# Kernel tuning notes

Measured on AMD Instinct MI355X. Metric: run time of the kernel, lower is better.

Reference implementation:

```python
import jax, jax.numpy as jnp
import numpy as np


def setup_inputs() -> dict:
    key = jax.random.key(0)
    k1, k2, k3, k4, k5 = jax.random.split(key, 5)
    C, S = 256, 16  # in_channels, se_channels
    x = jax.random.normal(k1, (64, C, 56, 56), dtype=jnp.float32)
    # 1x1 conv weights stored as [out, in] (kernel spatial dims are 1x1)
    w1 = jax.random.normal(k2, (S, C), dtype=jnp.float32) * (1.0 / np.sqrt(C))
    b1 = jax.random.normal(k3, (S,), dtype=jnp.float32) * 0.01
    w2 = jax.random.normal(k4, (C, S), dtype=jnp.float32) * (1.0 / np.sqrt(S))
    b2 = jax.random.normal(k5, (C,), dtype=jnp.float32) * 0.01
    return {"x": x, "w1": w1, "b1": b1, "w2": w2, "b2": b2}


def reference(x, w1, b1, w2, b2):
    # squeeze: global average pool over H, W -> [N, C]
    s = jnp.mean(x, axis=(2, 3))
    # excitation: 1x1 conv MLP with swish then sigmoid gate
    h = jnp.einsum('nc,sc->ns', s, w1) + b1          # [N, S]
    h = h * jax.nn.sigmoid(h)                        # swish
    g = jax.nn.sigmoid(jnp.einsum('ns,cs->nc', h, w2) + b2)  # [N, C]
    # broadcast multiply back over spatial dims
    return x * g[:, :, None, None]
```

## Files before the change

### kernel.cpp

```cpp
#include <hip/hip_runtime.h>
#include <math.h>

#define N_   64
#define C_   256
#define S_   16
#define HW_  3136
#define HW4_ 784
#define ROWS_ (N_ * C_)
#define BLK_  4096

typedef float f32x4 __attribute__((ext_vector_type(4)));

__device__ __forceinline__ float sigmoidf_(float v) {
    return 1.0f / (1.0f + expf(-v));
}

__global__ __launch_bounds__(256) void se_pool(const float* __restrict__ x,
                                               float* __restrict__ s) {
    const int wave = threadIdx.x >> 6;
    const int lane = threadIdx.x & 63;
    const int row  = blockIdx.x * 4 + wave;
    const f32x4* xr = reinterpret_cast<const f32x4*>(x + (size_t)row * HW_);

    f32x4 acc = {0.f, 0.f, 0.f, 0.f};
    #pragma unroll
    for (int u = 0; u < 12; ++u) acc += xr[lane + 64 * u];
    float sum = (acc.x + acc.y) + (acc.z + acc.w);
    if (lane < 16) {
        f32x4 v = xr[768 + lane];
        sum += (v.x + v.y) + (v.z + v.w);
    }
    #pragma unroll
    for (int off = 32; off; off >>= 1) sum += __shfl_down(sum, off, 64);
    if (lane == 0) s[row] = sum * (1.0f / (float)HW_);
}

__global__ __launch_bounds__(256) void se_mlp(const float* __restrict__ s,
                                              const float* __restrict__ w1,
                                              const float* __restrict__ b1,
                                              const float* __restrict__ w2,
                                              const float* __restrict__ b2,
                                              float* __restrict__ g) {
    const int n = blockIdx.x;
    const int t = threadIdx.x;
    __shared__ float s_sh[C_];
    __shared__ float h_sh[S_];
    s_sh[t] = s[n * C_ + t];
    __syncthreads();

    const int j  = t >> 4;
    const int sl = t & 15;
    float p = 0.f;
    #pragma unroll
    for (int k = sl; k < C_; k += 16) p += s_sh[k] * w1[j * C_ + k];
    #pragma unroll
    for (int m = 8; m; m >>= 1) p += __shfl_xor(p, m, 64);
    if (sl == 0) {
        float hv = p + b1[j];
        h_sh[j] = hv * sigmoidf_(hv);
    }
    __syncthreads();

    float acc = b2[t];
    #pragma unroll
    for (int k = 0; k < S_; ++k) acc += h_sh[k] * w2[t * S_ + k];
    g[n * C_ + t] = sigmoidf_(acc);
}

__global__ __launch_bounds__(256) void se_scale(const float* __restrict__ x,
                                                const float* __restrict__ g,
                                                float* __restrict__ out) {
    const int wave = threadIdx.x >> 6;
    const int lane = threadIdx.x & 63;
    const int row  = blockIdx.x * 4 + wave;
    const float gv = g[row];
    const f32x4* xr = reinterpret_cast<const f32x4*>(x + (size_t)row * HW_);
    f32x4* orow = reinterpret_cast<f32x4*>(out + (size_t)row * HW_);

    #pragma unroll
    for (int u = 0; u < 12; ++u) {
        f32x4 v = xr[lane + 64 * u];
        v *= gv;
        __builtin_nontemporal_store(v, &orow[lane + 64 * u]);
    }
    if (lane < 16) {
        f32x4 v = xr[768 + lane];
        v *= gv;
        __builtin_nontemporal_store(v, &orow[768 + lane]);
    }
}

extern "C" void kernel_launch(void* const* d_in, const int* in_sizes, int n_in,
                              void* d_out, int out_size, void* d_ws, size_t ws_size,
                              hipStream_t stream) {
    const float* x  = (const float*)d_in[0];
    const float* w1 = (const float*)d_in[1];
    const float* b1 = (const float*)d_in[2];
    const float* w2 = (const float*)d_in[3];
    const float* b2 = (const float*)d_in[4];
    float* out = (float*)d_out;

    float* s = (float*)d_ws;
    float* g = s + ROWS_;

    se_pool <<<BLK_, 256, 0, stream>>>(x, s);
    se_mlp  <<<N_,   256, 0, stream>>>(s, w1, b1, w2, b2, g);
    se_scale<<<BLK_, 256, 0, stream>>>(x, g, out);
}
```

Baseline: 99.91 us.

## Fuse SE excitation MLP into scale kernel, recomputing gate per wave

Removes the separate small MLP kernel by having each wave in the scale kernel recompute the gate for its (n,c) row from the pooled vector, w1, and w2 with shuffle reductions. The x loads are issued into registers before the MLP math so their latency overlaps the gate computation. This eliminates one kernel launch and the serialization of a low-occupancy 64-block kernel. In exchange, every wave redundantly computes the full 16x256 first layer, which adds ALU work, L2 traffic for s and w1, and register pressure from holding 13 vectors of x.

Result: slower. 112.4 us (+12.5%).

```diff
diff --git a/kernel.cpp b/kernel.cpp
--- a/kernel.cpp
+++ b/kernel.cpp
@@ -35,57 +35,53 @@
     if (lane == 0) s[row] = sum * (1.0f / (float)HW_);
 }
 
-__global__ __launch_bounds__(256) void se_mlp(const float* __restrict__ s,
-                                              const float* __restrict__ w1,
-                                              const float* __restrict__ b1,
-                                              const float* __restrict__ w2,
-                                              const float* __restrict__ b2,
-                                              float* __restrict__ g) {
-    const int n = blockIdx.x;
-    const int t = threadIdx.x;
-    __shared__ float s_sh[C_];
-    __shared__ float h_sh[S_];
-    s_sh[t] = s[n * C_ + t];
-    __syncthreads();
-
-    const int j  = t >> 4;
-    const int sl = t & 15;
-    float p = 0.f;
-    #pragma unroll
-    for (int k = sl; k < C_; k += 16) p += s_sh[k] * w1[j * C_ + k];
-    #pragma unroll
-    for (int m = 8; m; m >>= 1) p += __shfl_xor(p, m, 64);
-    if (sl == 0) {
-        float hv = p + b1[j];
-        h_sh[j] = hv * sigmoidf_(hv);
-    }
-    __syncthreads();
-
-    float acc = b2[t];
-    #pragma unroll
-    for (int k = 0; k < S_; ++k) acc += h_sh[k] * w2[t * S_ + k];
-    g[n * C_ + t] = sigmoidf_(acc);
-}
-
-__global__ __launch_bounds__(256) void se_scale(const float* __restrict__ x,
-                                                const float* __restrict__ g,
-                                                float* __restrict__ out) {
+__global__ __launch_bounds__(256) void se_gate_scale(
+    const float* __restrict__ x, const float* __restrict__ s,
+    const float* __restrict__ w1, const float* __restrict__ b1,
+    const float* __restrict__ w2, const float* __restrict__ b2,
+    float* __restrict__ out)
+{
     const int wave = threadIdx.x >> 6;
     const int lane = threadIdx.x & 63;
     const int row  = blockIdx.x * 4 + wave;
-    const float gv = g[row];
+    const int n    = row >> 8;
+    const int c    = row & (C_ - 1);
     const f32x4* xr = reinterpret_cast<const f32x4*>(x + (size_t)row * HW_);
+
+    f32x4 xv[12];
+    #pragma unroll
+    for (int u = 0; u < 12; ++u) xv[u] = xr[lane + 64 * u];
+    f32x4 xt = {0.f, 0.f, 0.f, 0.f};
+    if (lane < 16) xt = xr[768 + lane];
+
+    const int j   = lane >> 2;
+    const int seg = lane & 3;
+    const f32x4* s4 = reinterpret_cast<const f32x4*>(s  + n * C_ + seg * 64);
+    const f32x4* w4 = reinterpret_cast<const f32x4*>(w1 + j * C_ + seg * 64);
+    f32x4 pa = {0.f, 0.f, 0.f, 0.f};
+    #pragma unroll
+    for (int m = 0; m < 16; ++m) pa += s4[m] * w4[m];
+    float p = (pa.x + pa.y) + (pa.z + pa.w);
+    p += __shfl_xor(p, 1, 64);
+    p += __shfl_xor(p, 2, 64);
+    float hv = p + b1[j];
+    hv = hv * sigmoidf_(hv);
+
+    float term = (seg == 0) ? hv * w2[c * S_ + j] : 0.f;
+    term += __shfl_xor(term, 4,  64);
+    term += __shfl_xor(term, 8,  64);
+    term += __shfl_xor(term, 16, 64);
+    term += __shfl_xor(term, 32, 64);
+    const float gv = sigmoidf_(__shfl(term, 0, 64) + b2[c]);
+
     f32x4* orow = reinterpret_cast<f32x4*>(out + (size_t)row * HW_);
-
     #pragma unroll
     for (int u = 0; u < 12; ++u) {
-        f32x4 v = xr[lane + 64 * u];
-        v *= gv;
+        f32x4 v = xv[u] * gv;
         __builtin_nontemporal_store(v, &orow[lane + 64 * u]);
     }
     if (lane < 16) {
-        f32x4 v = xr[768 + lane];
-        v *= gv;
+        f32x4 v = xt * gv;
         __builtin_nontemporal_store(v, &orow[768 + lane]);
     }
 }
@@ -101,9 +97,7 @@
     float* out = (float*)d_out;
 
     float* s = (float*)d_ws;
-    float* g = s + ROWS_;
 
-    se_pool <<<BLK_, 256, 0, stream>>>(x, s);
-    se_mlp  <<<N_,   256, 0, stream>>>(s, w1, b1, w2, b2, g);
-    se_scale<<<BLK_, 256, 0, stream>>>(x, g, out);
+    se_pool      <<<BLK_, 256, 0, stream>>>(x, s);
+    se_gate_scale<<<BLK_, 256, 0, stream>>>(x, s, w1, b1, w2, b2, out);
 }
```

## Fuse second SE linear layer and sigmoid gate into the scale kernel

Applied to the files above, without the earlier changes.

The MLP kernel is split. A single-block kernel now computes only the hidden swish activations for all 64x16 outputs using vectorized dot products. The second linear layer, bias and sigmoid are computed per row inside the scale kernel with a 16-lane shuffle reduction. This shrinks the serial middle kernel, but the scale kernel now does extra gate arithmetic and small loads before streaming x, and the one-block kernel has little parallelism.

Measured after the change: 126.2 us. +26.3%, slower.

```diff
diff --git a/kernel.cpp b/kernel.cpp
--- a/kernel.cpp
+++ b/kernel.cpp
@@ -35,48 +35,47 @@
     if (lane == 0) s[row] = sum * (1.0f / (float)HW_);
 }
 
-__global__ __launch_bounds__(256) void se_mlp(const float* __restrict__ s,
-                                              const float* __restrict__ w1,
-                                              const float* __restrict__ b1,
-                                              const float* __restrict__ w2,
-                                              const float* __restrict__ b2,
-                                              float* __restrict__ g) {
-    const int n = blockIdx.x;
+__global__ __launch_bounds__(256) void se_h(const float* __restrict__ s,
+                                            const float* __restrict__ w1,
+                                            const float* __restrict__ b1,
+                                            float* __restrict__ h) {
     const int t = threadIdx.x;
-    __shared__ float s_sh[C_];
-    __shared__ float h_sh[S_];
-    s_sh[t] = s[n * C_ + t];
-    __syncthreads();
-
-    const int j  = t >> 4;
-    const int sl = t & 15;
-    float p = 0.f;
     #pragma unroll
-    for (int k = sl; k < C_; k += 16) p += s_sh[k] * w1[j * C_ + k];
-    #pragma unroll
-    for (int m = 8; m; m >>= 1) p += __shfl_xor(p, m, 64);
-    if (sl == 0) {
-        float hv = p + b1[j];
-        h_sh[j] = hv * sigmoidf_(hv);
+    for (int i = 0; i < 4; ++i) {
+        const int d = t * 4 + i;
+        const int n = d >> 4;
+        const int j = d & 15;
+        const f32x4* s4 = reinterpret_cast<const f32x4*>(s  + n * C_);
+        const f32x4* w4 = reinterpret_cast<const f32x4*>(w1 + j * C_);
+        f32x4 pa = {0.f, 0.f, 0.f, 0.f};
+        #pragma unroll
+        for (int m = 0; m < 64; ++m) pa += s4[m] * w4[m];
+        float p = (pa.x + pa.y) + (pa.z + pa.w) + b1[j];
+        h[d] = p * sigmoidf_(p);
     }
-    __syncthreads();
-
-    float acc = b2[t];
-    #pragma unroll
-    for (int k = 0; k < S_; ++k) acc += h_sh[k] * w2[t * S_ + k];
-    g[n * C_ + t] = sigmoidf_(acc);
 }
 
 __global__ __launch_bounds__(256) void se_scale(const float* __restrict__ x,
-                                                const float* __restrict__ g,
+                                                const float* __restrict__ h,
+                                                const float* __restrict__ w2,
+                                                const float* __restrict__ b2,
                                                 float* __restrict__ out) {
     const int wave = threadIdx.x >> 6;
     const int lane = threadIdx.x & 63;
     const int row  = blockIdx.x * 4 + wave;
-    const float gv = g[row];
+    const int n    = row >> 8;
+    const int c    = row & (C_ - 1);
+
+    const int j = lane & 15;
+    float term = h[n * S_ + j] * w2[c * S_ + j];
+    term += __shfl_xor(term, 1, 64);
+    term += __shfl_xor(term, 2, 64);
+    term += __shfl_xor(term, 4, 64);
+    term += __shfl_xor(term, 8, 64);
+    const float gv = sigmoidf_(term + b2[c]);
+
     const f32x4* xr = reinterpret_cast<const f32x4*>(x + (size_t)row * HW_);
     f32x4* orow = reinterpret_cast<f32x4*>(out + (size_t)row * HW_);
-
     #pragma unroll
     for (int u = 0; u < 12; ++u) {
         f32x4 v = xr[lane + 64 * u];
@@ -101,9 +100,9 @@
     float* out = (float*)d_out;
 
     float* s = (float*)d_ws;
-    float* g = s + ROWS_;
+    float* h = s + ROWS_;
 
     se_pool <<<BLK_, 256, 0, stream>>>(x, s);
-    se_mlp  <<<N_,   256, 0, stream>>>(s, w1, b1, w2, b2, g);
-    se_scale<<<BLK_, 256, 0, stream>>>(x, g, out);
+    se_h    <<<1,    256, 0, stream>>>(s, w1, b1, h);
+    se_scale<<<BLK_, 256, 0, stream>>>(x, h, w2, b2, out);
 }
```
